# Kernel optimization log

Measured on AMD Instinct MI355X. Metric: run time of the kernel, lower is better.

Reference implementation:

```python
import jax, jax.numpy as jnp
import numpy as np

B, S, D, H = 4, 2048, 1024, 16
HD = D // H


def setup_inputs() -> dict:
    key = jax.random.key(0)
    ks = jax.random.split(key, 12)
    scale = 1.0 / np.sqrt(D)
    inp = {
        "query": jax.random.normal(ks[0], (B, S, D), jnp.float32),
        "key_": jax.random.normal(ks[1], (B, S, D), jnp.float32),
        "value": jax.random.normal(ks[2], (B, S, D), jnp.float32),
        "Wq": jax.random.normal(ks[3], (D, D), jnp.float32) * scale,
        "bq": jnp.zeros((D,), jnp.float32),
        "Wk": jax.random.normal(ks[4], (D, D), jnp.float32) * scale,
        "bk": jnp.zeros((D,), jnp.float32),
        "Wv": jax.random.normal(ks[5], (D, D), jnp.float32) * scale,
        "bv": jnp.zeros((D,), jnp.float32),
        "Wo": jax.random.normal(ks[6], (D, D), jnp.float32) * scale,
        "bo": jnp.zeros((D,), jnp.float32),
        # causal mask: 1 where attention allowed, 0 where masked (masked_fill(mask==0, -inf))
        "mask": jnp.tril(jnp.ones((S, S), jnp.int32))[None, None, :, :],
    }
    return inp


def reference(query, key_, value, Wq, bq, Wk, bk, Wv, bv, Wo, bo, mask):
    def split_heads(x):  # [B,S,D] -> [B,H,S,HD]
        return x.reshape(B, S, H, HD).transpose(0, 2, 1, 3)

    Q = split_heads(query @ Wq.T + bq)
    K = split_heads(key_ @ Wk.T + bk)
    V = split_heads(value @ Wv.T + bv)

    scores = jnp.einsum("bhqd,bhkd->bhqk", Q, K) / np.sqrt(HD).astype(np.float32)
    scores = jnp.where(mask == 0, -jnp.inf, scores)
    attn = jax.nn.softmax(scores, axis=-1)  # [B,H,S,S]
    out = jnp.einsum("bhqk,bhkd->bhqd", attn, V)  # [B,H,S,HD]
    concat = out.transpose(0, 2, 1, 3).reshape(B, S, D)
    return concat @ Wo.T + bo
```

## Files before the change

kernel.cpp:

```cpp
#include <hip/hip_runtime.h>
#include <hip/hip_bf16.h>
#include <math.h>

#define BB 4
#define SS 2048
#define DD 1024
#define HH 16
#define HD 64

#define NEG_BIG (-1e30f)


typedef short v8s __attribute__((ext_vector_type(8)));
typedef float v4f __attribute__((ext_vector_type(4)));

__device__ inline unsigned cvt_pk_bf16(float lo, float hi) {
    unsigned r;
    asm("v_cvt_pk_bf16_f32 %0, %1, %2" : "=v"(r) : "v"(lo), "v"(hi));
    return r;
}

__device__ inline short f2bf(float f) {
    return (short)cvt_pk_bf16(f, f);
}

__device__ inline v4f v4f_zero() {
    v4f z;
    z[0] = 0.f; z[1] = 0.f; z[2] = 0.f; z[3] = 0.f;
    return z;
}

__device__ inline v8s load8f(const float* p) {
    v4f a = *(const v4f*)p;
    v4f b = *(const v4f*)(p + 4);
    union { unsigned u[4]; v8s s; } x;
    x.u[0] = cvt_pk_bf16(a[0], a[1]);
    x.u[1] = cvt_pk_bf16(a[2], a[3]);
    x.u[2] = cvt_pk_bf16(b[0], b[1]);
    x.u[3] = cvt_pk_bf16(b[2], b[3]);
    return x.s;
}

__device__ inline void gll16(const void* g, void* l) {
    __builtin_amdgcn_global_load_lds(
        (const __attribute__((address_space(1))) unsigned*)g,
        (__attribute__((address_space(3))) unsigned*)l, 16, 0, 0);
}

__global__ __launch_bounds__(256) void conv_bf16_kernel(
    const float* __restrict__ in, short* __restrict__ out, int n8) {
    int i = blockIdx.x * 256 + threadIdx.x;
    const int stride = gridDim.x * 256;
    for (; i < n8; i += stride) {
        *((v8s*)out + i) = load8f(in + (size_t)i * 8);
    }
}

template <int MODE>
__global__ __launch_bounds__(256) void gemm_kernel(
    const void* __restrict__ Pbig, const float* __restrict__ Psml,
    const float* __restrict__ Pbias, void* __restrict__ PC,
    const void* __restrict__ Pbig2, const float* __restrict__ Psml2,
    const float* __restrict__ Pbias2, void* __restrict__ PC2) {
    __shared__ short sA[128 * 32];
    __shared__ short sB[128 * 32];

    const int tid = threadIdx.x;
    const int lane = tid & 63;
    const int wave = tid >> 6;
    const int quad = lane >> 4;
    const int l16 = lane & 15;
    const int wm = wave >> 1;
    const int wn = wave & 1;

    const void* Big = Pbig;
    const float* Sml = Psml;
    const float* bias = Pbias;
    void* Cv = PC;
    if (MODE == 0 && blockIdx.z == 1) {
        Big = Pbig2; Sml = Psml2; bias = Pbias2; Cv = PC2;
    }

    int bx = blockIdx.x, by = blockIdx.y;
    if (MODE != 1) {
        int b = bx + (by << 3);
        int l = ((b & 7) << 6) + (b >> 3);
        bx = l & 7;
        by = l >> 3;
    }
    const int m0 = by * 128;
    const int n0 = bx * 128;

    short* sBig = (MODE == 1) ? sB : sA;
    short* sSml = (MODE == 1) ? sA : sB;
    const int grow = (wave << 5) + (lane >> 2);
    const int gcol = (lane & 3) << 3;
    const short* BigS = (const short*)Big;
    size_t gbase0, gbase1;
    if (MODE == 3) {
        int ma = m0 + grow, mb = m0 + grow + 16;
        gbase0 = ((size_t)((ma >> 11) * HH) * SS + (ma & 2047)) * HD;
        gbase1 = ((size_t)((mb >> 11) * HH) * SS + (mb & 2047)) * HD;
    } else {
        int r0 = ((MODE == 1) ? n0 : m0) + grow;
        gbase0 = (size_t)r0 * 1024 + gcol;
        gbase1 = gbase0 + (size_t)16 * 1024;
    }
    short* ldst0 = sBig + (wave << 10);
    short* ldst1 = ldst0 + 512;

    const int sml_base = (MODE == 1) ? m0 : n0;

    v4f acc[4][4];
#pragma unroll
    for (int i = 0; i < 4; i++)
#pragma unroll
        for (int j = 0; j < 4; j++) acc[i][j] = v4f_zero();

    for (int k0 = 0; k0 < 1024; k0 += 32) {
        __syncthreads();
        if (MODE == 3) {
            size_t hoff = (size_t)(k0 >> 6) * (SS * HD) + (k0 & 63) + gcol;
            gll16(BigS + gbase0 + hoff, ldst0);
            gll16(BigS + gbase1 + hoff, ldst1);
        } else {
            gll16(BigS + gbase0 + k0, ldst0);
            gll16(BigS + gbase1 + k0, ldst1);
        }
#pragma unroll
        for (int p = 0; p < 2; p++) {
            int idx = ((p << 8) + tid) << 3;
            int r = idx >> 5;
            int c = idx & 31;
            *(v8s*)&sSml[idx] =
                load8f(Sml + (size_t)(sml_base + r) * 1024 + k0 + c);
        }
        __syncthreads();

        v8s af[4], bfr[4];
#pragma unroll
        for (int i = 0; i < 4; i++)
            af[i] = *(const v8s*)&sA[(wm * 64 + i * 16 + l16) * 32 + quad * 8];
#pragma unroll
        for (int j = 0; j < 4; j++)
            bfr[j] = *(const v8s*)&sB[(wn * 64 + j * 16 + l16) * 32 + quad * 8];
#pragma unroll
        for (int i = 0; i < 4; i++)
#pragma unroll
            for (int j = 0; j < 4; j++)
                acc[i][j] = __builtin_amdgcn_mfma_f32_16x16x32_bf16(
                    af[i], bfr[j], acc[i][j], 0, 0, 0);
    }

#pragma unroll
    for (int i = 0; i < 4; i++) {
#pragma unroll
        for (int j = 0; j < 4; j++) {
#pragma unroll
            for (int r = 0; r < 4; r++) {
                int ml = wm * 64 + i * 16 + quad * 4 + r;
                int nl = wn * 64 + j * 16 + l16;
                int m = m0 + ml;
                int n = n0 + nl;
                float v = acc[i][j][r];
                if (MODE == 0) {
                    v += bias[n];
                    int b = m >> 11, s = m & 2047, h = n >> 6, d = n & 63;
                    ((short*)Cv)[(((size_t)(b * HH + h) * SS + s) << 6) + d] =
                        f2bf(v);
                } else if (MODE == 1) {
                    v += bias[m];
                    int h = m >> 6, d = m & 63, b = n >> 11, s = n & 2047;
                    ((short*)Cv)[((size_t)(b * HH + h) * HD + d) * SS + s] =
                        f2bf(v);
                } else {
                    v += bias[n];
                    ((float*)Cv)[(size_t)m * 1024 + n] = v;
                }
            }
        }
    }
}

__global__ __launch_bounds__(256) void attn_kernel(
    short* __restrict__ QO, const short* __restrict__ Kt,
    const short* __restrict__ Vt) {
    constexpr int LDR = 64 + 8;
    __shared__ short sK[64 * LDR];
    __shared__ short sV[64 * LDR];
    __shared__ short sP[4][16 * LDR];

    const int tid = threadIdx.x;
    const int lane = tid & 63;
    const int wave = tid >> 6;
    const int quad = lane >> 4;
    const int l16 = lane & 15;
    const int qt = (int)gridDim.x - 1 - (int)blockIdx.x;
    const int bh = blockIdx.y;

    short* Qh = QO + (size_t)bh * SS * HD;
    const short* Kh = Kt + (size_t)bh * SS * HD;
    const short* Vh = Vt + (size_t)bh * HD * SS;

    const int qrow = qt * 64 + wave * 16 + l16;
    v8s qf[2];
    qf[0] = *(const v8s*)&Qh[(size_t)qrow * HD + quad * 8];
    qf[1] = *(const v8s*)&Qh[(size_t)qrow * HD + 32 + quad * 8];

    v8s onesb;
#pragma unroll
    for (int i = 0; i < 8; i++) onesb[i] = (short)0x3F80;

    v4f o[4];
#pragma unroll
    for (int j = 0; j < 4; j++) o[j] = v4f_zero();
    v4f oSum = v4f_zero();
    float mOld[4];
#pragma unroll
    for (int r = 0; r < 4; r++) mOld[r] = NEG_BIG;

    const int qg_base = qt * 64 + wave * 16 + quad * 4;

    for (int kt = 0; kt <= qt; kt++) {
        __syncthreads();
#pragma unroll
        for (int p = 0; p < 2; p++) {
            int idx = (p * 256 + tid) * 8;
            int r = idx >> 6;
            int c = idx & 63;
            *(v8s*)&sK[r * LDR + c] =
                *(const v8s*)&Kh[(size_t)(kt * 64 + r) * HD + c];
            *(v8s*)&sV[r * LDR + c] =
                *(const v8s*)&Vh[(size_t)r * SS + kt * 64 + c];
        }
        __syncthreads();

        __builtin_amdgcn_s_setprio(1);
        v4f sc[4];
#pragma unroll
        for (int j = 0; j < 4; j++) {
            v8s b0 = *(const v8s*)&sK[(j * 16 + l16) * LDR + quad * 8];
            v8s b1 = *(const v8s*)&sK[(j * 16 + l16) * LDR + 32 + quad * 8];
            v4f t = __builtin_amdgcn_mfma_f32_16x16x32_bf16(qf[0], b0,
                                                            v4f_zero(), 0, 0, 0);
            sc[j] = __builtin_amdgcn_mfma_f32_16x16x32_bf16(qf[1], b1, t, 0, 0, 0);
        }
        __builtin_amdgcn_s_setprio(0);

        float x[4][4];
        const bool diag = (kt == qt);
#pragma unroll
        for (int j = 0; j < 4; j++) {
#pragma unroll
            for (int r = 0; r < 4; r++) {
                float v = sc[j][r] * 0.125f;
                if (diag) {
                    int kg = kt * 64 + j * 16 + l16;
                    int qg = qg_base + r;
                    if (kg > qg) v = NEG_BIG;
                }
                x[j][r] = v;
            }
        }

        float mNew[4], alpha[4];
#pragma unroll
        for (int r = 0; r < 4; r++) {
            float t = fmaxf(fmaxf(x[0][r], x[1][r]), fmaxf(x[2][r], x[3][r]));
#pragma unroll
            for (int off = 8; off >= 1; off >>= 1) t = fmaxf(t, __shfl_xor(t, off));
            mNew[r] = fmaxf(mOld[r], t);
            alpha[r] = __expf(mOld[r] - mNew[r]);
            mOld[r] = mNew[r];
        }

        short* Pw = sP[wave];
#pragma unroll
        for (int j = 0; j < 4; j++)
#pragma unroll
            for (int r = 0; r < 4; r++) {
                float p = __expf(x[j][r] - mNew[r]);
                Pw[(quad * 4 + r) * LDR + j * 16 + l16] = f2bf(p);
            }
#pragma unroll
        for (int j = 0; j < 4; j++)
#pragma unroll
            for (int r = 0; r < 4; r++) o[j][r] *= alpha[r];
#pragma unroll
        for (int r = 0; r < 4; r++) oSum[r] *= alpha[r];

        v8s pa0 = *(const v8s*)&Pw[l16 * LDR + quad * 8];
        v8s pa1 = *(const v8s*)&Pw[l16 * LDR + 32 + quad * 8];
        __builtin_amdgcn_s_setprio(1);
#pragma unroll
        for (int j = 0; j < 4; j++) {
            v8s v0 = *(const v8s*)&sV[(j * 16 + l16) * LDR + quad * 8];
            v8s v1 = *(const v8s*)&sV[(j * 16 + l16) * LDR + 32 + quad * 8];
            o[j] = __builtin_amdgcn_mfma_f32_16x16x32_bf16(pa0, v0, o[j], 0, 0, 0);
            o[j] = __builtin_amdgcn_mfma_f32_16x16x32_bf16(pa1, v1, o[j], 0, 0, 0);
        }
        oSum = __builtin_amdgcn_mfma_f32_16x16x32_bf16(pa0, onesb, oSum, 0, 0, 0);
        oSum = __builtin_amdgcn_mfma_f32_16x16x32_bf16(pa1, onesb, oSum, 0, 0, 0);
        __builtin_amdgcn_s_setprio(0);
    }

#pragma unroll
    for (int r = 0; r < 4; r++) {
        float inv = 1.f / oSum[r];
        int s = qg_base + r;
#pragma unroll
        for (int j = 0; j < 4; j++) {
            float v = o[j][r] * inv;
            Qh[(size_t)s * HD + j * 16 + l16] = f2bf(v);
        }
    }
}

extern "C" void kernel_launch(void* const* d_in, const int* in_sizes, int n_in,
                              void* d_out, int out_size, void* d_ws, size_t ws_size,
                              hipStream_t stream) {
    const float* query = (const float*)d_in[0];
    const float* key_ = (const float*)d_in[1];
    const float* value = (const float*)d_in[2];
    const float* Wq = (const float*)d_in[3];
    const float* bq = (const float*)d_in[4];
    const float* Wk = (const float*)d_in[5];
    const float* bk = (const float*)d_in[6];
    const float* Wv = (const float*)d_in[7];
    const float* bv = (const float*)d_in[8];
    const float* Wo = (const float*)d_in[9];
    const float* bo = (const float*)d_in[10];
    float* out = (float*)d_out;

    const size_t NE = (size_t)BB * SS * DD;

    short* qx = (short*)d_out;
    short* kx = (short*)d_out + NE;
    short* vx = (short*)d_out + NE;
    short* vw = (short*)d_out;
    short* qw = (short*)d_ws;
    short* kw = (short*)d_ws + NE;

    dim3 blk(256);
    const int n8 = (int)(NE / 8);
    conv_bf16_kernel<<<dim3(2048), blk, 0, stream>>>(query, qx, n8);
    conv_bf16_kernel<<<dim3(2048), blk, 0, stream>>>(key_, kx, n8);
    gemm_kernel<0><<<dim3(8, 64, 2), blk, 0, stream>>>(
        qx, Wq, bq, qw, kx, Wk, bk, kw);
    conv_bf16_kernel<<<dim3(2048), blk, 0, stream>>>(value, vx, n8);
    gemm_kernel<1><<<dim3(64, 8), blk, 0, stream>>>(
        vx, Wv, bv, vw, nullptr, nullptr, nullptr, nullptr);
    attn_kernel<<<dim3(SS / 64, BB * HH), blk, 0, stream>>>(qw, kw, vw);
    gemm_kernel<3><<<dim3(8, 64), blk, 0, stream>>>(
        qw, Wo, bo, out, nullptr, nullptr, nullptr, nullptr);
}
```

Measured before the change: 508.7 us.

## Pre-convert weights to bf16 and stage both GEMM operands via direct LDS loads

```diff
diff --git a/kernel.cpp b/kernel.cpp
--- a/kernel.cpp
+++ b/kernel.cpp
@@ -30,9 +30,7 @@
     return z;
 }
 
-__device__ inline v8s load8f(const float* p) {
-    v4f a = *(const v4f*)p;
-    v4f b = *(const v4f*)(p + 4);
+__device__ inline v8s cvt8(v4f a, v4f b) {
     union { unsigned u[4]; v8s s; } x;
     x.u[0] = cvt_pk_bf16(a[0], a[1]);
     x.u[1] = cvt_pk_bf16(a[2], a[3]);
@@ -41,6 +39,10 @@
     return x.s;
 }
 
+__device__ inline v8s load8f(const float* p) {
+    return cvt8(*(const v4f*)p, *(const v4f*)(p + 4));
+}
+
 __device__ inline void gll16(const void* g, void* l) {
     __builtin_amdgcn_global_load_lds(
         (const __attribute__((address_space(1))) unsigned*)g,
@@ -58,10 +60,8 @@
 
 template <int MODE>
 __global__ __launch_bounds__(256) void gemm_kernel(
-    const void* __restrict__ Pbig, const float* __restrict__ Psml,
-    const float* __restrict__ Pbias, void* __restrict__ PC,
-    const void* __restrict__ Pbig2, const float* __restrict__ Psml2,
-    const float* __restrict__ Pbias2, void* __restrict__ PC2) {
+    const void* __restrict__ Av, const void* __restrict__ Bv,
+    const float* __restrict__ bias, void* __restrict__ Cv) {
     __shared__ short sA[128 * 32];
     __shared__ short sB[128 * 32];
 
@@ -73,43 +73,46 @@
     const int wm = wave >> 1;
     const int wn = wave & 1;
 
-    const void* Big = Pbig;
-    const float* Sml = Psml;
-    const float* bias = Pbias;
-    void* Cv = PC;
-    if (MODE == 0 && blockIdx.z == 1) {
-        Big = Pbig2; Sml = Psml2; bias = Pbias2; Cv = PC2;
-    }
-
-    int bx = blockIdx.x, by = blockIdx.y;
+    int bx, by;
     if (MODE != 1) {
-        int b = bx + (by << 3);
+        int b = blockIdx.x + (blockIdx.y << 3);
         int l = ((b & 7) << 6) + (b >> 3);
         bx = l & 7;
         by = l >> 3;
+    } else {
+        bx = blockIdx.x;
+        by = blockIdx.y;
     }
     const int m0 = by * 128;
     const int n0 = bx * 128;
 
-    short* sBig = (MODE == 1) ? sB : sA;
-    short* sSml = (MODE == 1) ? sA : sB;
     const int grow = (wave << 5) + (lane >> 2);
     const int gcol = (lane & 3) << 3;
-    const short* BigS = (const short*)Big;
-    size_t gbase0, gbase1;
+    const int ldoff = wave << 10;
+
+    const short* As = (const short*)Av;
+    size_t gaA0, gaA1;
     if (MODE == 3) {
         int ma = m0 + grow, mb = m0 + grow + 16;
-        gbase0 = ((size_t)((ma >> 11) * HH) * SS + (ma & 2047)) * HD;
-        gbase1 = ((size_t)((mb >> 11) * HH) * SS + (mb & 2047)) * HD;
+        gaA0 = ((size_t)((ma >> 11) * HH) * SS + (ma & 2047)) * HD;
+        gaA1 = ((size_t)((mb >> 11) * HH) * SS + (mb & 2047)) * HD;
     } else {
-        int r0 = ((MODE == 1) ? n0 : m0) + grow;
-        gbase0 = (size_t)r0 * 1024 + gcol;
-        gbase1 = gbase0 + (size_t)16 * 1024;
-    }
-    short* ldst0 = sBig + (wave << 10);
-    short* ldst1 = ldst0 + 512;
-
-    const int sml_base = (MODE == 1) ? m0 : n0;
+        gaA0 = (size_t)(m0 + grow) * 1024 + gcol;
+        gaA1 = gaA0 + (size_t)16 * 1024;
+    }
+
+    const short* Bs = (const short*)Bv;
+    const float* Bf = (const float*)Bv;
+    size_t gaB0 = 0, gaB1 = 0;
+    if (MODE != 1) {
+        gaB0 = (size_t)(n0 + grow) * 1024 + gcol;
+        gaB1 = gaB0 + (size_t)16 * 1024;
+    }
+    const int idx0 = tid << 3, idx1 = (256 + tid) << 3;
+    const float* Bsrc0 = (MODE == 1)
+        ? Bf + (size_t)(n0 + (idx0 >> 5)) * 1024 + (idx0 & 31) : nullptr;
+    const float* Bsrc1 = (MODE == 1)
+        ? Bf + (size_t)(n0 + (idx1 >> 5)) * 1024 + (idx1 & 31) : nullptr;
 
     v4f acc[4][4];
 #pragma unroll
@@ -121,19 +124,18 @@
         __syncthreads();
         if (MODE == 3) {
             size_t hoff = (size_t)(k0 >> 6) * (SS * HD) + (k0 & 63) + gcol;
-            gll16(BigS + gbase0 + hoff, ldst0);
-            gll16(BigS + gbase1 + hoff, ldst1);
+            gll16(As + gaA0 + hoff, sA + ldoff);
+            gll16(As + gaA1 + hoff, sA + ldoff + 512);
         } else {
-            gll16(BigS + gbase0 + k0, ldst0);
-            gll16(BigS + gbase1 + k0, ldst1);
-        }
-#pragma unroll
-        for (int p = 0; p < 2; p++) {
-            int idx = ((p << 8) + tid) << 3;
-            int r = idx >> 5;
-            int c = idx & 31;
-            *(v8s*)&sSml[idx] =
-                load8f(Sml + (size_t)(sml_base + r) * 1024 + k0 + c);
+            gll16(As + gaA0 + k0, sA + ldoff);
+            gll16(As + gaA1 + k0, sA + ldoff + 512);
+        }
+        if (MODE == 1) {
+            *(v8s*)&sB[idx0] = load8f(Bsrc0 + k0);
+            *(v8s*)&sB[idx1] = load8f(Bsrc1 + k0);
+        } else {
+            gll16(Bs + gaB0 + k0, sB + ldoff);
+            gll16(Bs + gaB1 + k0, sB + ldoff + 512);
         }
         __syncthreads();
 
@@ -333,24 +335,31 @@
     float* out = (float*)d_out;
 
     const size_t NE = (size_t)BB * SS * DD;
-
-    short* qx = (short*)d_out;
-    short* kx = (short*)d_out + NE;
-    short* vx = (short*)d_out + NE;
-    short* vw = (short*)d_out;
-    short* qw = (short*)d_ws;
-    short* kw = (short*)d_ws + NE;
+    const size_t WE = (size_t)DD * DD;
+
+    short* qx  = (short*)d_out;
+    short* kx  = (short*)d_out + NE;
+    short* wqb = (short*)d_ws + NE;
+    short* wkb = (short*)d_out;
+    short* wvb = (short*)d_out + WE;
+    short* vw  = (short*)d_out + NE;
+    short* qw  = (short*)d_ws;
+    short* kw  = (short*)d_ws + NE;
+    short* wob = (short*)d_ws + NE;
 
     dim3 blk(256);
-    const int n8 = (int)(NE / 8);
-    conv_bf16_kernel<<<dim3(2048), blk, 0, stream>>>(query, qx, n8);
-    conv_bf16_kernel<<<dim3(2048), blk, 0, stream>>>(key_, kx, n8);
-    gemm_kernel<0><<<dim3(8, 64, 2), blk, 0, stream>>>(
-        qx, Wq, bq, qw, kx, Wk, bk, kw);
-    conv_bf16_kernel<<<dim3(2048), blk, 0, stream>>>(value, vx, n8);
-    gemm_kernel<1><<<dim3(64, 8), blk, 0, stream>>>(
-        vx, Wv, bv, vw, nullptr, nullptr, nullptr, nullptr);
+    const int n8a = (int)(NE / 8);
+    const int n8w = (int)(WE / 8);
+
+    conv_bf16_kernel<<<dim3(2048), blk, 0, stream>>>(query, qx, n8a);
+    conv_bf16_kernel<<<dim3(2048), blk, 0, stream>>>(key_, kx, n8a);
+    conv_bf16_kernel<<<dim3(512), blk, 0, stream>>>(Wq, wqb, n8w);
+    gemm_kernel<0><<<dim3(8, 64), blk, 0, stream>>>(qx, wqb, bq, qw);
+    conv_bf16_kernel<<<dim3(512), blk, 0, stream>>>(Wk, wkb, n8w);
+    gemm_kernel<0><<<dim3(8, 64), blk, 0, stream>>>(kx, wkb, bk, kw);
+    conv_bf16_kernel<<<dim3(512), blk, 0, stream>>>(Wv, wvb, n8w);
+    gemm_kernel<1><<<dim3(64, 8), blk, 0, stream>>>(wvb, value, bv, vw);
     attn_kernel<<<dim3(SS / 64, BB * HH), blk, 0, stream>>>(qw, kw, vw);
-    gemm_kernel<3><<<dim3(8, 64), blk, 0, stream>>>(
-        qw, Wo, bo, out, nullptr, nullptr, nullptr, nullptr);
-}
+    conv_bf16_kernel<<<dim3(512), blk, 0, stream>>>(Wo, wob, n8w);
+    gemm_kernel<3><<<dim3(8, 64), blk, 0, stream>>>(qw, wob, bo, out);
+}
```

After: 475.2 us. 6.6% less time.
